# Kernel tuning notes

Hardware: AMD Instinct MI355X
Metric: run time of the kernel (lower is better)

## Reference

```python
import jax, jax.numpy as jnp
import numpy as np
import math

B, S, H, NH = 2, 2048, 1024, 16
HD = H // NH


def setup_inputs() -> dict:
    key = jax.random.key(0)
    k1, k2, k3 = jax.random.split(key, 3)
    hidden_states = jax.random.normal(k1, (B, S, H), dtype=jnp.float32)
    attention_mask = jnp.zeros((B, 1, 1, S), dtype=jnp.float32)
    w_qkv = jax.random.normal(k2, (3 * H, H), dtype=jnp.float32) * (1.0 / math.sqrt(H))
    w_out = jax.random.normal(k3, (H, H), dtype=jnp.float32) * (1.0 / math.sqrt(H))
    gate = jnp.ones((NH,), dtype=jnp.float32)
    return {"hidden_states": hidden_states, "attention_mask": attention_mask,
            "w_qkv": w_qkv, "w_out": w_out, "gate": gate}


def reference(hidden_states, attention_mask, w_qkv, w_out, gate):
    b, s, h = hidden_states.shape
    nh, hd = NH, HD
    # fused QKV projection (no bias)
    qkv = hidden_states @ w_qkv.T                      # [b, s, 3h]
    qkv = qkv.reshape(b, s, 3, nh, hd)
    q, k, v = jnp.moveaxis(qkv, 2, 0)                  # each [b, s, nh, hd]
    q = q.transpose(0, 2, 1, 3)                        # [b, nh, s, hd]
    k = k.transpose(0, 2, 1, 3)
    v = v.transpose(0, 2, 1, 3)
    scores = jnp.einsum('bhqd,bhkd->bhqk', q, k) / math.sqrt(hd)
    scores = scores + attention_mask                   # broadcast [b,1,1,s]
    probs = jax.nn.softmax(scores, axis=-1)            # dropout p=0 -> identity
    ctx = jnp.einsum('bhqk,bhkd->bhqd', probs, v)      # [b, nh, s, hd]
    ctx = ctx.transpose(0, 2, 1, 3)                    # [b, s, nh, hd]
    ctx = ctx * gate[None, None, :, None]              # per-head gating
    ctx = ctx.reshape(b, s, h)
    out = ctx @ w_out.T
    # all gates active (> 1e-4) -> active_gates/num_heads == 1, no rescale
    return out
```

## Files before the change

### kernel.cpp

```cpp
#include <hip/hip_runtime.h>
#include <stdint.h>


typedef __attribute__((ext_vector_type(8))) short short8;
typedef __attribute__((ext_vector_type(4))) float floatx4;
typedef __attribute__((ext_vector_type(4))) unsigned int uint4v;
typedef __attribute__((ext_vector_type(2))) unsigned int uint2v;

__device__ __forceinline__ unsigned short f2bf(float f) {
    unsigned int u = __float_as_uint(f);
    unsigned int r = u + 0x7fffu + ((u >> 16) & 1u);
    return (unsigned short)(r >> 16);
}
#if __has_builtin(__builtin_amdgcn_cvt_pk_bf16_f32)
__device__ __forceinline__ unsigned int pack_bf2(float lo, float hi) {
    auto v = __builtin_amdgcn_cvt_pk_bf16_f32(lo, hi);
    return __builtin_bit_cast(unsigned int, v);
}
#else
__device__ __forceinline__ unsigned int pack_bf2(float lo, float hi) {
    unsigned int a = __float_as_uint(lo) + 0x8000u;
    unsigned int b = __float_as_uint(hi) + 0x8000u;
    return __builtin_amdgcn_perm(b, a, 0x07060302u);
}
#endif

#if __has_builtin(__builtin_amdgcn_exp2f)
#define EXP2(x) __builtin_amdgcn_exp2f(x)
#else
#define EXP2(x) exp2f(x)
#endif

__device__ __forceinline__ void gl2lds16(const void* g, void* l) {
    __builtin_amdgcn_global_load_lds(
        (const __attribute__((address_space(1))) unsigned int*)g,
        (__attribute__((address_space(3))) unsigned int*)l, 16, 0, 0);
}

#define MFMA32(a, b, c) __builtin_amdgcn_mfma_f32_16x16x32_bf16((a), (b), (c), 0, 0, 0)

__global__ __launch_bounds__(256)
void cvt_all(const float* __restrict__ a, const float* __restrict__ b,
             const float* __restrict__ c, const float* __restrict__ mask,
             unsigned short* __restrict__ oa, unsigned short* __restrict__ ob,
             unsigned short* __restrict__ oc, float* __restrict__ m2b)
{
    int i = blockIdx.x * 256 + threadIdx.x;
    if (i >= 2097152) {
        int off = i - 2097152;
        float4 v = *(const float4*)(mask + (size_t)off * 4);
        const float L2E = 1.44269504f, C2 = -14.4269504f;
        float4 w;
        w.x = fmaf(v.x, L2E, C2); w.y = fmaf(v.y, L2E, C2);
        w.z = fmaf(v.z, L2E, C2); w.w = fmaf(v.w, L2E, C2);
        *(float4*)(m2b + (size_t)off * 4) = w;
        return;
    }
    const float* src; unsigned short* dst; int off;
    if (i < 1048576)      { src = a; dst = oa; off = i; }
    else if (i < 1835008) { src = b; dst = ob; off = i - 1048576; }
    else                  { src = c; dst = oc; off = i - 1835008; }
    float4 v = *(const float4*)(src + (size_t)off * 4);
    uint2v w;
    w[0] = pack_bf2(v.x, v.y);
    w[1] = pack_bf2(v.z, v.w);
    *(uint2v*)(dst + (size_t)off * 4) = w;
}

template<int MODE, int BN>
__global__ __launch_bounds__(256)
void gemm_nt(const unsigned short* __restrict__ A,
             const unsigned short* __restrict__ Bm,
             unsigned short* __restrict__ out0,
             unsigned short* __restrict__ out1,
             unsigned short* __restrict__ out2,
             float* __restrict__ outf,
             int N)
{
    __shared__ unsigned char smem[16384 + BN * 128];
    const int K = 1024;
    const int BSL = BN / 32;
    const int tid  = threadIdx.x;
    const int wave = tid >> 6, lane = tid & 63;
    const int l15  = lane & 15, quad = lane >> 4;
    const int wm = wave >> 1, wn = wave & 1;

    int Lid = blockIdx.y * gridDim.x + blockIdx.x;
    int bm = (Lid & 7) * 4 + ((Lid >> 3) & 3);
    int bn = Lid >> 5;

    floatx4 acc[4][BSL];
#pragma unroll
    for (int i = 0; i < 4; i++)
#pragma unroll
        for (int j = 0; j < BSL; j++)
            acc[i][j] = floatx4{0.f, 0.f, 0.f, 0.f};

    int soffA[4], soffB[BSL];
#pragma unroll
    for (int l = 0; l < 4; l++) {
        int s = (wave * 4 + l) * 64 + lane;
        int row = s >> 3;
        soffA[l] = row * K + (((s & 7) ^ (row & 7)) * 8);
    }
#pragma unroll
    for (int l = 0; l < BSL; l++) {
        int s = (wave * BSL + l) * 64 + lane;
        int row = s >> 3;
        soffB[l] = row * K + (((s & 7) ^ (row & 7)) * 8);
    }

    const unsigned short* Abase = A  + (size_t)(bm * 128) * K;
    const unsigned short* Bbase = Bm + (size_t)(bn * BN) * K;

    for (int k0 = 0; k0 < K; k0 += 64) {
        __syncthreads();
#pragma unroll
        for (int l = 0; l < 4; l++)
            gl2lds16(Abase + (size_t)soffA[l] + k0, &smem[(wave * 4 + l) * 1024]);
#pragma unroll
        for (int l = 0; l < BSL; l++)
            gl2lds16(Bbase + (size_t)soffB[l] + k0, &smem[16384 + (wave * BSL + l) * 1024]);
        __syncthreads();
#pragma unroll
        for (int s2 = 0; s2 < 2; s2++) {
            short8 af[4], bfr[BSL];
            int c = s2 * 4 + quad;
#pragma unroll
            for (int i = 0; i < 4; i++) {
                int row = wm * 64 + i * 16 + l15;
                af[i] = *(const short8*)(&smem[row * 128 + ((c ^ (row & 7)) * 16)]);
            }
#pragma unroll
            for (int j = 0; j < BSL; j++) {
                int row = wn * (BN / 2) + j * 16 + l15;
                bfr[j] = *(const short8*)(&smem[16384 + row * 128 + ((c ^ (row & 7)) * 16)]);
            }
#pragma unroll
            for (int i = 0; i < 4; i++)
#pragma unroll
                for (int j = 0; j < BSL; j++)
                    acc[i][j] = MFMA32(af[i], bfr[j], acc[i][j]);
        }
    }

#pragma unroll
    for (int i = 0; i < 4; i++) {
#pragma unroll
        for (int j = 0; j < BSL; j++) {
            int n = bn * BN + wn * (BN / 2) + j * 16 + l15;
#pragma unroll
            for (int r = 0; r < 4; r++) {
                int m = bm * 128 + wm * 64 + i * 16 + quad * 4 + r;
                float fv = acc[i][j][r];
                if (MODE == 1) {
                    outf[(size_t)m * N + n] = fv;
                } else {
                    int t = n >> 10;
                    int h = (n >> 6) & 15;
                    int d = n & 63;
                    int b = m >> 11, si = m & 2047;
                    if (t == 2) {
                        int sip = (si & ~31) | (((si >> 2) & 3) << 3)
                                | (((si >> 4) & 1) << 2) | (si & 3);
                        out2[(((size_t)(b * 16 + h)) * 64 + d) * 2048 + sip] = f2bf(fv);
                    } else {
                        size_t off = (((size_t)(b * 16 + h)) * 2048 + si) * 64 + d;
                        unsigned short* dst = (t == 0) ? out0 : out1;
                        dst[off] = f2bf(fv);
                    }
                }
            }
        }
    }
}

__global__ __launch_bounds__(256, 2)
void attn_kernel(const unsigned short* __restrict__ Qb,
                 const unsigned short* __restrict__ Kb,
                 const unsigned short* __restrict__ VbT,
                 const float* __restrict__ m2b,
                 const float* __restrict__ gateb,
                 unsigned short* __restrict__ ctx)
{
    __shared__ unsigned char smem[65536];
    const int S = 2048;
    const int tid  = threadIdx.x;
    const int wave = tid >> 6, lane = tid & 63;
    const int l15  = lane & 15, quad = lane >> 4;

    int Lid = blockIdx.y * gridDim.x + blockIdx.x;
    int bh = (Lid & 7) * 4 + ((Lid >> 3) & 3);
    int qc = Lid >> 5;
    const int b = bh >> 4, h = bh & 15;
    const int q0 = qc * 64;

    const size_t headoff = (size_t)bh * S * 64;
    const unsigned short* Qh  = Qb  + headoff;
    const unsigned short* Kh  = Kb  + headoff;
    const unsigned short* VhT = VbT + headoff;
    const float* m2p = m2b + (size_t)b * S;

    const int WB = wave * 16384;

    short8 aq[4][2];
#pragma unroll
    for (int sub = 0; sub < 4; sub++)
#pragma unroll
        for (int s2 = 0; s2 < 2; s2++)
            aq[sub][s2] = *(const short8*)(Qh + (size_t)(q0 + sub * 16 + l15) * 64 + s2 * 32 + quad * 8);

    floatx4 o[4][4];
    floatx4 lq[4];
#pragma unroll
    for (int sub = 0; sub < 4; sub++) {
        lq[sub] = floatx4{0.f, 0.f, 0.f, 0.f};
#pragma unroll
        for (int dt = 0; dt < 4; dt++) o[sub][dt] = floatx4{0.f, 0.f, 0.f, 0.f};
    }

    int koff[4], voff[4];
#pragma unroll
    for (int l = 0; l < 4; l++) {
        int s = l * 64 + lane;
        int key = s >> 3;
        koff[l] = key * 64 + (((s & 7) ^ (key & 7)) * 8);
        int d = s >> 2;
        voff[l] = d * 2048 + (((s & 3) ^ (d & 3)) * 8);
    }
    int qkoff[2];
#pragma unroll
    for (int s2 = 0; s2 < 2; s2++)
        qkoff[s2] = l15 * 128 + (((s2 * 4 + quad) ^ (l15 & 7)) * 16);
    const int pvoff = 4096 + l15 * 64 + ((quad ^ (l15 & 3)) * 16);

    const float C1 = 0.18033688f;
    const uint4v onesu = {0x3F803F80u, 0x3F803F80u, 0u, 0u};
    const short8 ONES = __builtin_bit_cast(short8, onesu);
    const floatx4 FZ = {0.f, 0.f, 0.f, 0.f};

    {
        const unsigned short* kg = Kh + (size_t)(wave * 32) * 64;
        const unsigned short* vg = VhT + wave * 32;
#pragma unroll
        for (int l = 0; l < 4; l++) {
            gl2lds16(kg + koff[l], &smem[WB + l * 1024]);
            gl2lds16(vg + voff[l], &smem[WB + 4096 + l * 1024]);
        }
    }

    for (int i = 0; i < 16; i++) {
        const int kb = (wave + 4 * i) * 32;
        float4 mf[2];
#pragma unroll
        for (int t = 0; t < 2; t++)
            mf[t] = *(const float4*)(m2p + kb + t * 16 + quad * 4);
        asm volatile("" ::: "memory");
        {
            const int kbn = (wave + 4 * ((i + 1) & 15)) * 32;
            const int hb = WB + ((i + 1) & 1) * 8192;
            const unsigned short* kg = Kh + (size_t)kbn * 64;
            const unsigned short* vg = VhT + kbn;
#pragma unroll
            for (int l = 0; l < 4; l++) {
                gl2lds16(kg + koff[l], &smem[hb + l * 1024]);
                gl2lds16(vg + voff[l], &smem[hb + 4096 + l * 1024]);
            }
        }
        asm volatile("s_waitcnt vmcnt(8)" ::: "memory");

        const int cb = WB + (i & 1) * 8192;
        uint4v vfu[4];
#pragma unroll
        for (int dt = 0; dt < 4; dt++)
            vfu[dt] = *(const uint4v*)(&smem[cb + pvoff + dt * 1024]);
        short8 kf[2][2];
#pragma unroll
        for (int t = 0; t < 2; t++)
#pragma unroll
            for (int s2 = 0; s2 < 2; s2++)
                kf[t][s2] = *(const short8*)(&smem[cb + qkoff[s2] + t * 2048]);

#pragma unroll
        for (int sub = 0; sub < 4; sub++) {
            floatx4 st[2];
            st[0] = MFMA32(kf[0][0], aq[sub][0], FZ);
            st[1] = MFMA32(kf[1][0], aq[sub][0], FZ);
            st[0] = MFMA32(kf[0][1], aq[sub][1], st[0]);
            st[1] = MFMA32(kf[1][1], aq[sub][1], st[1]);
#pragma unroll
            for (int t = 0; t < 2; t++) {
                float e0 = EXP2(fmaf(st[t][0], C1, mf[t].x));
                float e1 = EXP2(fmaf(st[t][1], C1, mf[t].y));
                float e2 = EXP2(fmaf(st[t][2], C1, mf[t].z));
                float e3 = EXP2(fmaf(st[t][3], C1, mf[t].w));
                uint4v pu = {pack_bf2(e0, e1), pack_bf2(e2, e3), 0u, 0u};
                short8 pf = __builtin_bit_cast(short8, pu);
#pragma unroll
                for (int dt = 0; dt < 4; dt++) {
                    uint4v vu = {vfu[dt][t * 2], vfu[dt][t * 2 + 1], 0u, 0u};
                    short8 va = __builtin_bit_cast(short8, vu);
                    o[sub][dt] = MFMA32(va, pf, o[sub][dt]);
                }
                lq[sub] = MFMA32(ONES, pf, lq[sub]);
            }
        }
    }

    asm volatile("s_waitcnt vmcnt(0)" ::: "memory");

    floatx4 ro[4];
#pragma unroll
    for (int ph = 0; ph < 2; ph++) {
        __syncthreads();
#pragma unroll
        for (int sub = 0; sub < 4; sub++)
#pragma unroll
            for (int d2 = 0; d2 < 2; d2++)
                *(floatx4*)(&smem[(((wave * 4 + sub) * 2 + d2) * 64 + lane) * 16]) = o[sub][ph * 2 + d2];
        __syncthreads();
#pragma unroll
        for (int d2 = 0; d2 < 2; d2++) {
            floatx4 acc = floatx4{0.f, 0.f, 0.f, 0.f};
#pragma unroll
            for (int w2 = 0; w2 < 4; w2++)
                acc += *(const floatx4*)(&smem[(((w2 * 4 + wave) * 2 + d2) * 64 + lane) * 16]);
            ro[ph * 2 + d2] = acc;
        }
    }
    __syncthreads();
#pragma unroll
    for (int sub = 0; sub < 4; sub++)
        *(floatx4*)(&smem[((wave * 4 + sub) * 64 + lane) * 16]) = lq[sub];
    __syncthreads();
    floatx4 rl = floatx4{0.f, 0.f, 0.f, 0.f};
#pragma unroll
    for (int w2 = 0; w2 < 4; w2++)
        rl += *(const floatx4*)(&smem[((w2 * 4 + wave) * 64 + lane) * 16]);

    float iv = gateb[h] / rl[0];
    size_t base = ((size_t)(b * 2048 + q0 + wave * 16 + l15)) * 1024 + h * 64 + quad * 4;
#pragma unroll
    for (int dt = 0; dt < 4; dt++) {
        uint2v w;
        w[0] = pack_bf2(ro[dt][0] * iv, ro[dt][1] * iv);
        w[1] = pack_bf2(ro[dt][2] * iv, ro[dt][3] * iv);
        *(uint2v*)(ctx + base + dt * 16) = w;
    }
}

extern "C" void kernel_launch(void* const* d_in, const int* in_sizes, int n_in,
                              void* d_out, int out_size, void* d_ws, size_t ws_size,
                              hipStream_t stream)
{
    const float* hidden = (const float*)d_in[0];
    const float* mask   = (const float*)d_in[1];
    const float* w_qkv  = (const float*)d_in[2];
    const float* w_out  = (const float*)d_in[3];
    const float* gate   = (const float*)d_in[4];
    float* out = (float*)d_out;

    unsigned short* q_buf = (unsigned short*)d_ws;
    unsigned short* k_buf = q_buf + 4194304;
    unsigned short* v_buf = k_buf + 4194304;
    unsigned short* c_buf = v_buf + 4194304;
    unsigned short* h_bf  = c_buf + 4194304;
    unsigned short* wq_bf = h_bf  + 4194304;
    unsigned short* wo_bf = wq_bf + 3145728;
    float* m2_buf = (float*)(wo_bf + 1048576);

    cvt_all<<<8196, 256, 0, stream>>>(hidden, w_qkv, w_out, mask,
                                      h_bf, wq_bf, wo_bf, m2_buf);

    gemm_nt<0, 128><<<dim3(24, 32), 256, 0, stream>>>(h_bf, wq_bf, q_buf, k_buf, v_buf, nullptr, 3072);
    attn_kernel<<<dim3(32, 32), 256, 0, stream>>>(q_buf, k_buf, v_buf, m2_buf, gate, c_buf);
    gemm_nt<1, 64><<<dim3(16, 32), 256, 0, stream>>>(c_buf, wo_bf, nullptr, nullptr, nullptr, out, 1024);
}
```

Before: 202.2 us.

## Fold softmax scale into Q projection and merge PV MFMAs over full K=32

The QKV GEMM epilogue now pre-multiplies Q by the log2-scaled softmax constant, so the attention inner loop no longer needs an fma per score. The mask bias is passed as the MFMA accumulator input instead of being added afterwards. The two half-filled PV MFMAs per sub-tile (zero-padded K=16) become one full-K MFMA using all eight bf16 lanes, which halves PV and row-sum MFMA count. Pre-scaling Q before bf16 rounding slightly changes numerics.

```diff
diff --git a/kernel.cpp b/kernel.cpp
--- a/kernel.cpp
+++ b/kernel.cpp
@@ -165,6 +165,7 @@
                                 | (((si >> 4) & 1) << 2) | (si & 3);
                         out2[(((size_t)(b * 16 + h)) * 64 + d) * 2048 + sip] = f2bf(fv);
                     } else {
+                        if (t == 0) fv *= 0.18033688f;
                         size_t off = (((size_t)(b * 16 + h)) * 2048 + si) * 64 + d;
                         unsigned short* dst = (t == 0) ? out0 : out1;
                         dst[off] = f2bf(fv);
@@ -234,10 +235,8 @@
         qkoff[s2] = l15 * 128 + (((s2 * 4 + quad) ^ (l15 & 7)) * 16);
     const int pvoff = 4096 + l15 * 64 + ((quad ^ (l15 & 3)) * 16);
 
-    const float C1 = 0.18033688f;
-    const uint4v onesu = {0x3F803F80u, 0x3F803F80u, 0u, 0u};
+    const uint4v onesu = {0x3F803F80u, 0x3F803F80u, 0x3F803F80u, 0x3F803F80u};
     const short8 ONES = __builtin_bit_cast(short8, onesu);
-    const floatx4 FZ = {0.f, 0.f, 0.f, 0.f};
 
     {
         const unsigned short* kg = Kh + (size_t)(wave * 32) * 64;
@@ -251,10 +250,10 @@
 
     for (int i = 0; i < 16; i++) {
         const int kb = (wave + 4 * i) * 32;
-        float4 mf[2];
+        floatx4 mf[2];
 #pragma unroll
         for (int t = 0; t < 2; t++)
-            mf[t] = *(const float4*)(m2p + kb + t * 16 + quad * 4);
+            mf[t] = *(const floatx4*)(m2p + kb + t * 16 + quad * 4);
         asm volatile("" ::: "memory");
         {
             const int kbn = (wave + 4 * ((i + 1) & 15)) * 32;
@@ -270,10 +269,10 @@
         asm volatile("s_waitcnt vmcnt(8)" ::: "memory");
 
         const int cb = WB + (i & 1) * 8192;
-        uint4v vfu[4];
+        short8 vf[4];
 #pragma unroll
         for (int dt = 0; dt < 4; dt++)
-            vfu[dt] = *(const uint4v*)(&smem[cb + pvoff + dt * 1024]);
+            vf[dt] = *(const short8*)(&smem[cb + pvoff + dt * 1024]);
         short8 kf[2][2];
 #pragma unroll
         for (int t = 0; t < 2; t++)
@@ -283,27 +282,21 @@
 
 #pragma unroll
         for (int sub = 0; sub < 4; sub++) {
-            floatx4 st[2];
-            st[0] = MFMA32(kf[0][0], aq[sub][0], FZ);
-            st[1] = MFMA32(kf[1][0], aq[sub][0], FZ);
-            st[0] = MFMA32(kf[0][1], aq[sub][1], st[0]);
-            st[1] = MFMA32(kf[1][1], aq[sub][1], st[1]);
-#pragma unroll
-            for (int t = 0; t < 2; t++) {
-                float e0 = EXP2(fmaf(st[t][0], C1, mf[t].x));
-                float e1 = EXP2(fmaf(st[t][1], C1, mf[t].y));
-                float e2 = EXP2(fmaf(st[t][2], C1, mf[t].z));
-                float e3 = EXP2(fmaf(st[t][3], C1, mf[t].w));
-                uint4v pu = {pack_bf2(e0, e1), pack_bf2(e2, e3), 0u, 0u};
-                short8 pf = __builtin_bit_cast(short8, pu);
-#pragma unroll
-                for (int dt = 0; dt < 4; dt++) {
-                    uint4v vu = {vfu[dt][t * 2], vfu[dt][t * 2 + 1], 0u, 0u};
-                    short8 va = __builtin_bit_cast(short8, vu);
-                    o[sub][dt] = MFMA32(va, pf, o[sub][dt]);
-                }
-                lq[sub] = MFMA32(ONES, pf, lq[sub]);
-            }
+            floatx4 st0 = MFMA32(kf[0][0], aq[sub][0], mf[0]);
+            floatx4 st1 = MFMA32(kf[1][0], aq[sub][0], mf[1]);
+            st0 = MFMA32(kf[0][1], aq[sub][1], st0);
+            st1 = MFMA32(kf[1][1], aq[sub][1], st1);
+            float e00 = EXP2(st0[0]), e01 = EXP2(st0[1]);
+            float e02 = EXP2(st0[2]), e03 = EXP2(st0[3]);
+            float e10 = EXP2(st1[0]), e11 = EXP2(st1[1]);
+            float e12 = EXP2(st1[2]), e13 = EXP2(st1[3]);
+            uint4v pu = {pack_bf2(e00, e01), pack_bf2(e02, e03),
+                         pack_bf2(e10, e11), pack_bf2(e12, e13)};
+            short8 pf = __builtin_bit_cast(short8, pu);
+#pragma unroll
+            for (int dt = 0; dt < 4; dt++)
+                o[sub][dt] = MFMA32(vf[dt], pf, o[sub][dt]);
+            lq[sub] = MFMA32(ONES, pf, lq[sub]);
         }
     }
 
```

New measurement: 193.3 us. -4.4%, faster.
